# Kernel optimization log

Hardware: AMD Instinct MI355X
Metric: run time of the kernel (lower is better)

The kernel has to match this reference:

```python
import jax, jax.numpy as jnp
import numpy as np
from jax import lax

DIVISOR = 2.0

def setup_inputs() -> dict:
    key = jax.random.key(0)
    k1, k2, k3, k4 = jax.random.split(key, 4)
    x = jax.random.normal(k1, (32, 3, 32, 128, 128), dtype=jnp.float16)
    conv_w = jax.random.normal(k2, (16, 3, 3, 3, 3), dtype=jnp.float16) * 0.1
    conv_b = jax.random.normal(k3, (16,), dtype=jnp.float16)
    bias = jax.random.normal(k4, (16,), dtype=jnp.float16)
    return {"x": x, "conv_w": conv_w, "conv_b": conv_b, "bias": bias}

def reference(x, conv_w, conv_b, bias):
    # Conv3d (valid padding, stride 1), fp16 like conv.half()
    y = lax.conv_general_dilated(
        x, conv_w, window_strides=(1, 1, 1), padding="VALID",
        dimension_numbers=("NCDHW", "OIDHW", "NCDHW"))
    y = y + conv_b[None, :, None, None, None]
    # Fused ReLU + 2x2x2 max pool
    y = jnp.maximum(y, jnp.asarray(0, y.dtype))
    B, C, D, H, W = y.shape
    Dp, Hp, Wp = D // 2, H // 2, W // 2
    pooled = y[:, :, :2 * Dp, :2 * Hp, :2 * Wp].reshape(
        B, C, Dp, 2, Hp, 2, Wp, 2).max(axis=(3, 5, 7))  # [B,C,Dp,Hp,Wp]
    # Spatial mean in fp32 (kernel accumulates in float)
    avg = pooled.astype(jnp.float32).mean(axis=(2, 3, 4))  # [B,C]
    # /divisor + bias[c], then sum over channels -> [B,1,1,1]
    per_ch = avg / DIVISOR + bias.astype(jnp.float32)[None, :]
    return per_ch.sum(axis=1).reshape(B, 1, 1, 1)
```

## Files before the change

### kernel.cpp

```cpp
#include <hip/hip_runtime.h>
#include <hip/hip_bf16.h>


typedef __attribute__((ext_vector_type(8)))  short  short8;
typedef __attribute__((ext_vector_type(4)))  float  floatx4;
typedef __attribute__((ext_vector_type(16))) float  floatx16;

__device__ __forceinline__ short f2bf(float f) {
    unsigned u = __builtin_bit_cast(unsigned, f);
    unsigned r = (u + 0x7FFFu + ((u >> 16) & 1u)) >> 16;
    return (short)r;
}

__device__ __forceinline__ unsigned pkbf2(float a, float b) {
    __hip_bfloat162 h = __float22bfloat162_rn(float2{a, b});
    unsigned r;
    __builtin_memcpy(&r, &h, 4);
    return r;
}

template <int CTRL>
__device__ __forceinline__ float dpp_max(float v) {
    int x = __builtin_bit_cast(int, v);
    int y = __builtin_amdgcn_mov_dpp(x, CTRL, 0xF, 0xF, true);
    return fmaxf(v, __builtin_bit_cast(float, y));
}

__global__ void init_kernel(const float* __restrict__ wg,
                            const float* __restrict__ biasg,
                            short* __restrict__ wtab,
                            float* __restrict__ out)
{
    const int t = threadIdx.x;
    if (t < 576) {
        const int lane = t & 63, f = t >> 6;
        const int kh = f / 3, kw = f % 3;
        const int m = lane & 31, hs = lane >> 5;
        const int dd = m >> 4, ch = m & 15;
        short8 v;
        #pragma unroll
        for (int j = 0; j < 8; ++j) {
            const int s = hs * 8 + j;
            const int dl = s >> 2, ci = s & 3;
            const int kd = dl - dd;
            v[j] = (ci < 3 && kd >= 0 && kd < 3)
                 ? f2bf(wg[ch * 81 + ci * 27 + kd * 9 + kh * 3 + kw]) : (short)0;
        }
        ((short8*)wtab)[f * 64 + lane] = v;
    }
    if (t < 32) {
        float s = 0.f;
        #pragma unroll
        for (int cc = 0; cc < 16; ++cc) s += biasg[cc];
        out[t] = s;
    }
}

__global__ __launch_bounds__(512, 4) void fused_conv_pool_reduce(
    const float* __restrict__ xg,
    const short* __restrict__ wtab,
    const float* __restrict__ cbg,
    float* __restrict__ out)
{
    __shared__ __align__(16) short rawT[2 * 130 * 64];
    __shared__ float wsums[8];

    const int hp  = blockIdx.x;
    const int b   = blockIdx.y;
    const int tid = threadIdx.x;
    const int lane = tid & 63;
    const int wv   = tid >> 6;
    const int hs   = lane >> 5;

    short8 af[9];
    #pragma unroll
    for (int f = 0; f < 9; ++f) af[f] = ((const short8*)wtab)[f * 64 + lane];
    float cb8[8];
    #pragma unroll
    for (int r = 0; r < 8; ++r) cb8[r] = cbg[(r & 3) + 8 * (r >> 2) + 4 * hs];

    if (tid < 64)
        *(unsigned long long*)((char*)rawT + (tid >> 5) * 16640 + 16384 + (tid & 31) * 8) = 0ULL;

    const int w4 = tid & 31, dr = (tid >> 5) & 3, hr = (tid >> 7) & 3;
    int waddr[4];
    {
        const int chunkL = hr * 2 + (dr >> 1);
        #pragma unroll
        for (int i = 0; i < 4; ++i) {
            const int row = 4 * w4 + i;
            const int phys = chunkL ^ ((row ^ (row >> 3)) & 7);
            waddr[i] = row * 128 + phys * 16 + (dr & 1) * 8;
        }
    }
    const int wi = (lane >> 1) & 15, hh = lane & 1;
    int raddr[3][3];
    #pragma unroll
    for (int kh = 0; kh < 3; ++kh) {
        #pragma unroll
        for (int kw = 0; kw < 3; ++kw) {
            const int row = wv * 16 + wi + kw;
            const int phys = ((hh + kh) * 2 + hs) ^ ((row ^ (row >> 3)) & 7);
            raddr[kh][kw] = row * 128 + phys * 16;
        }
    }

    const float* src = xg + ((size_t)b * 96 + dr) * 16384 + (2 * hp + hr) * 128 + 4 * w4;
    floatx4 c0 = *(const floatx4*)(src);
    floatx4 c1 = *(const floatx4*)(src + 524288);
    floatx4 c2 = *(const floatx4*)(src + 1048576);

    float vsum = 0.f;
    for (int dp = 0; dp < 15; ++dp) {
        const int bofs = (dp & 1) * 16640;
        #pragma unroll
        for (int i = 0; i < 4; ++i) {
            uint2 pk;
            pk.x = pkbf2(c0[i], c1[i]);
            pk.y = pkbf2(c2[i], 0.0f);
            *(uint2*)((char*)rawT + bofs + waddr[i]) = pk;
        }
        if (dp < 14) {
            src += 32768;
            c0 = *(const floatx4*)(src);
            c1 = *(const floatx4*)(src + 524288);
            c2 = *(const floatx4*)(src + 1048576);
        }
        __syncthreads();

        floatx16 acc = {0.f,0.f,0.f,0.f,0.f,0.f,0.f,0.f,
                        0.f,0.f,0.f,0.f,0.f,0.f,0.f,0.f};
        #pragma unroll
        for (int kh = 0; kh < 3; ++kh) {
            #pragma unroll
            for (int kw = 0; kw < 3; ++kw) {
                const short8 bf = *(const short8*)((char*)rawT + bofs + raddr[kh][kw]);
                acc = __builtin_amdgcn_mfma_f32_32x32x16_bf16(af[kh * 3 + kw], bf, acc, 0, 0, 0);
            }
        }
        #pragma unroll
        for (int r = 0; r < 8; ++r) {
            float v = fmaxf(fmaxf(acc[r], acc[r + 8]) + cb8[r], 0.f);
            v = dpp_max<0xB1>(v);
            v = dpp_max<0x4E>(v);
            vsum += v;
        }
    }

    const bool okl = ((lane & 3) == 0) && (wv * 16 + wi <= 124);
    float s = okl ? vsum : 0.f;
    #pragma unroll
    for (int off = 1; off < 64; off <<= 1) s += __shfl_xor(s, off, 64);

    if (lane == 0) wsums[wv] = s;
    __syncthreads();
    if (tid == 0) {
        float bs = 0.f;
        #pragma unroll
        for (int i = 0; i < 8; ++i) bs += wsums[i];
        atomicAdd(&out[b], bs * (1.0f / 119070.0f));
    }
}

extern "C" void kernel_launch(void* const* d_in, const int* in_sizes, int n_in,
                              void* d_out, int out_size, void* d_ws, size_t ws_size,
                              hipStream_t stream) {
    const float* x      = (const float*)d_in[0];
    const float* conv_w = (const float*)d_in[1];
    const float* conv_b = (const float*)d_in[2];
    const float* bias   = (const float*)d_in[3];
    float* out = (float*)d_out;
    short* wtab = (short*)d_ws;

    init_kernel<<<1, 576, 0, stream>>>(conv_w, bias, wtab, out);
    dim3 grid(63, 32);
    fused_conv_pool_reduce<<<grid, 512, 0, stream>>>(x, wtab, conv_b, out);
}
```

Before: 302.6 us.

## Deepen global prefetch to two slabs, use raw LDS barrier, remap block order

```diff
diff --git a/kernel.cpp b/kernel.cpp
--- a/kernel.cpp
+++ b/kernel.cpp
@@ -25,6 +25,8 @@
     int y = __builtin_amdgcn_mov_dpp(x, CTRL, 0xF, 0xF, true);
     return fmaxf(v, __builtin_bit_cast(float, y));
 }
+
+#define BAR() asm volatile("s_waitcnt lgkmcnt(0)\n\ts_barrier" ::: "memory")
 
 __global__ void init_kernel(const float* __restrict__ wg,
                             const float* __restrict__ biasg,
@@ -65,8 +67,11 @@
     __shared__ __align__(16) short rawT[2 * 130 * 64];
     __shared__ float wsums[8];
 
-    const int hp  = blockIdx.x;
-    const int b   = blockIdx.y;
+    const int lin = blockIdx.y * 63 + blockIdx.x;
+    const int nl  = (lin & 7) * 252 + (lin >> 3);
+    const int hp  = nl % 63;
+    const int b   = nl / 63;
+
     const int tid = threadIdx.x;
     const int lane = tid & 63;
     const int wv   = tid >> 6;
@@ -105,14 +110,9 @@
         }
     }
 
-    const float* src = xg + ((size_t)b * 96 + dr) * 16384 + (2 * hp + hr) * 128 + 4 * w4;
-    floatx4 c0 = *(const floatx4*)(src);
-    floatx4 c1 = *(const floatx4*)(src + 524288);
-    floatx4 c2 = *(const floatx4*)(src + 1048576);
-
     float vsum = 0.f;
-    for (int dp = 0; dp < 15; ++dp) {
-        const int bofs = (dp & 1) * 16640;
+
+    auto stage = [&](const floatx4& c0, const floatx4& c1, const floatx4& c2, int bofs) {
         #pragma unroll
         for (int i = 0; i < 4; ++i) {
             uint2 pk;
@@ -120,14 +120,8 @@
             pk.y = pkbf2(c2[i], 0.0f);
             *(uint2*)((char*)rawT + bofs + waddr[i]) = pk;
         }
-        if (dp < 14) {
-            src += 32768;
-            c0 = *(const floatx4*)(src);
-            c1 = *(const floatx4*)(src + 524288);
-            c2 = *(const floatx4*)(src + 1048576);
-        }
-        __syncthreads();
-
+    };
+    auto compute = [&](int bofs) {
         floatx16 acc = {0.f,0.f,0.f,0.f,0.f,0.f,0.f,0.f,
                         0.f,0.f,0.f,0.f,0.f,0.f,0.f,0.f};
         #pragma unroll
@@ -145,7 +139,40 @@
             v = dpp_max<0x4E>(v);
             vsum += v;
         }
-    }
+    };
+
+    const float* src = xg + ((size_t)b * 96 + dr) * 16384 + (2 * hp + hr) * 128 + 4 * w4;
+    floatx4 a0 = *(const floatx4*)(src);
+    floatx4 a1 = *(const floatx4*)(src + 524288);
+    floatx4 a2 = *(const floatx4*)(src + 1048576);
+    src += 32768;
+    floatx4 b0 = *(const floatx4*)(src);
+    floatx4 b1 = *(const floatx4*)(src + 524288);
+    floatx4 b2 = *(const floatx4*)(src + 1048576);
+    src += 32768;
+
+    for (int dpb = 0; dpb < 7; ++dpb) {
+        stage(a0, a1, a2, 0);
+        a0 = *(const floatx4*)(src);
+        a1 = *(const floatx4*)(src + 524288);
+        a2 = *(const floatx4*)(src + 1048576);
+        src += 32768;
+        BAR();
+        compute(0);
+
+        stage(b0, b1, b2, 16640);
+        if (dpb < 6) {
+            b0 = *(const floatx4*)(src);
+            b1 = *(const floatx4*)(src + 524288);
+            b2 = *(const floatx4*)(src + 1048576);
+            src += 32768;
+        }
+        BAR();
+        compute(16640);
+    }
+    stage(a0, a1, a2, 0);
+    BAR();
+    compute(0);
 
     const bool okl = ((lane & 3) == 0) && (wv * 16 + wi <= 124);
     float s = okl ? vsum : 0.f;
```

New measurement: 303.5 us. About the same (+0.3%).

## Swap MFMA operands, reorganize LDS ping-pong layout and remap block order

Applied to the files above, without the earlier changes.

```diff
diff --git a/kernel.cpp b/kernel.cpp
--- a/kernel.cpp
+++ b/kernel.cpp
@@ -3,6 +3,7 @@
 
 
 typedef __attribute__((ext_vector_type(8)))  short  short8;
+typedef __attribute__((ext_vector_type(2)))  float  floatx2;
 typedef __attribute__((ext_vector_type(4)))  float  floatx4;
 typedef __attribute__((ext_vector_type(16))) float  floatx16;
 
@@ -25,6 +26,10 @@
     int y = __builtin_amdgcn_mov_dpp(x, CTRL, 0xF, 0xF, true);
     return fmaxf(v, __builtin_bit_cast(float, y));
 }
+
+#define BAR() asm volatile("s_waitcnt lgkmcnt(0)\n\ts_barrier" ::: "memory")
+
+#define BUFSZ 16640
 
 __global__ void init_kernel(const float* __restrict__ wg,
                             const float* __restrict__ biasg,
@@ -36,7 +41,7 @@
         const int lane = t & 63, f = t >> 6;
         const int kh = f / 3, kw = f % 3;
         const int m = lane & 31, hs = lane >> 5;
-        const int dd = m >> 4, ch = m & 15;
+        const int ch = m >> 1, dd = m & 1;
         short8 v;
         #pragma unroll
         for (int j = 0; j < 8; ++j) {
@@ -65,8 +70,11 @@
     __shared__ __align__(16) short rawT[2 * 130 * 64];
     __shared__ float wsums[8];
 
-    const int hp  = blockIdx.x;
-    const int b   = blockIdx.y;
+    const int lin = blockIdx.y * 63 + blockIdx.x;
+    const int nl  = (lin & 7) * 252 + (lin >> 3);
+    const int hp  = nl % 63;
+    const int b   = nl / 63;
+
     const int tid = threadIdx.x;
     const int lane = tid & 63;
     const int wv   = tid >> 6;
@@ -75,24 +83,27 @@
     short8 af[9];
     #pragma unroll
     for (int f = 0; f < 9; ++f) af[f] = ((const short8*)wtab)[f * 64 + lane];
-    float cb8[8];
-    #pragma unroll
-    for (int r = 0; r < 8; ++r) cb8[r] = cbg[(r & 3) + 8 * (r >> 2) + 4 * hs];
+    const float cbv = cbg[(lane >> 1) & 15];
+    float maskA[4];
+    #pragma unroll
+    for (int a = 0; a < 4; ++a) {
+        const bool ok = ((lane & 1) == 0) && (wv * 8 + 2 * a + hs <= 62);
+        maskA[a] = ok ? 1.0f : 0.0f;
+    }
 
     if (tid < 64)
-        *(unsigned long long*)((char*)rawT + (tid >> 5) * 16640 + 16384 + (tid & 31) * 8) = 0ULL;
-
-    const int w4 = tid & 31, dr = (tid >> 5) & 3, hr = (tid >> 7) & 3;
-    int waddr[4];
-    {
-        const int chunkL = hr * 2 + (dr >> 1);
-        #pragma unroll
-        for (int i = 0; i < 4; ++i) {
-            const int row = 4 * w4 + i;
-            const int phys = chunkL ^ ((row ^ (row >> 3)) & 7);
-            waddr[i] = row * 128 + phys * 16 + (dr & 1) * 8;
-        }
-    }
+        *(unsigned long long*)((char*)rawT + (tid >> 5) * BUFSZ + 16384 + (tid & 31) * 8) = 0ULL;
+
+    #define SWZ(r) (((r) ^ ((r) >> 3)) & 7)
+
+    const int w4 = tid & 31, dr2 = (tid >> 5) & 1, rr = (tid >> 6) & 1, hr2 = (tid >> 7) & 3;
+    int waddr2[2];
+    #pragma unroll
+    for (int j = 0; j < 2; ++j) {
+        const int row = 2 * w4 + 64 * rr + j;
+        waddr2[j] = row * 128 + ((hr2 * 2) ^ SWZ(row)) * 16 + dr2 * 8;
+    }
+
     const int wi = (lane >> 1) & 15, hh = lane & 1;
     int raddr[3][3];
     #pragma unroll
@@ -100,33 +111,55 @@
         #pragma unroll
         for (int kw = 0; kw < 3; ++kw) {
             const int row = wv * 16 + wi + kw;
-            const int phys = ((hh + kh) * 2 + hs) ^ ((row ^ (row >> 3)) & 7);
+            const int phys = ((hh + kh) * 2 + hs) ^ SWZ(row);
             raddr[kh][kw] = row * 128 + phys * 16;
         }
     }
 
-    const float* src = xg + ((size_t)b * 96 + dr) * 16384 + (2 * hp + hr) * 128 + 4 * w4;
-    floatx4 c0 = *(const floatx4*)(src);
-    floatx4 c1 = *(const floatx4*)(src + 524288);
-    floatx4 c2 = *(const floatx4*)(src + 1048576);
-
-    float vsum = 0.f;
-    for (int dp = 0; dp < 15; ++dp) {
-        const int bofs = (dp & 1) * 16640;
+    {
+        const int w4p = tid & 31, drp = (tid >> 5) & 3, hrp = (tid >> 7) & 3;
+        const float* srcP = xg + ((size_t)b * 96 + drp) * 16384 + (2 * hp + hrp) * 128 + 4 * w4p;
+        const floatx4 c0 = *(const floatx4*)(srcP);
+        const floatx4 c1 = *(const floatx4*)(srcP + 524288);
+        const floatx4 c2 = *(const floatx4*)(srcP + 1048576);
+        const int chunkL = hrp * 2 + (drp >> 1);
         #pragma unroll
         for (int i = 0; i < 4; ++i) {
+            const int row = 4 * w4p + i;
+            const int ad = row * 128 + (chunkL ^ SWZ(row)) * 16 + (drp & 1) * 8;
             uint2 pk;
             pk.x = pkbf2(c0[i], c1[i]);
             pk.y = pkbf2(c2[i], 0.0f);
-            *(uint2*)((char*)rawT + bofs + waddr[i]) = pk;
-        }
-        if (dp < 14) {
-            src += 32768;
-            c0 = *(const floatx4*)(src);
-            c1 = *(const floatx4*)(src + 524288);
-            c2 = *(const floatx4*)(src + 1048576);
-        }
-        __syncthreads();
+            *(uint2*)((char*)rawT + ad) = pk;
+        }
+    }
+
+    const float* src2 = xg + ((size_t)b * 96 + 4 + dr2) * 16384
+                      + (2 * hp + hr2) * 128 + 2 * w4 + 64 * rr;
+    floatx2 A0 = *(const floatx2*)(src2);
+    floatx2 A1 = *(const floatx2*)(src2 + 524288);
+    floatx2 A2 = *(const floatx2*)(src2 + 1048576);
+
+    float vsum = 0.f;
+    for (int dp = 0; dp < 15; ++dp) {
+        const int p16 = (dp & 1) << 4;
+        if (dp <= 13) {
+            const int bw = (((dp >> 1) + 1) & 1) * BUFSZ;
+            uint2 pk0, pk1;
+            pk0.x = pkbf2(A0[0], A1[0]); pk0.y = pkbf2(A2[0], 0.0f);
+            pk1.x = pkbf2(A0[1], A1[1]); pk1.y = pkbf2(A2[1], 0.0f);
+            *(uint2*)((char*)rawT + bw + (waddr2[0] ^ p16)) = pk0;
+            *(uint2*)((char*)rawT + bw + (waddr2[1] ^ p16)) = pk1;
+            if (dp <= 12) {
+                src2 += 32768;
+                A0 = *(const floatx2*)(src2);
+                A1 = *(const floatx2*)(src2 + 524288);
+                A2 = *(const floatx2*)(src2 + 1048576);
+            }
+        }
+        BAR();
+
+        const int roff = (((dp + hs) >> 1) & 1) * BUFSZ;
 
         floatx16 acc = {0.f,0.f,0.f,0.f,0.f,0.f,0.f,0.f,
                         0.f,0.f,0.f,0.f,0.f,0.f,0.f,0.f};
@@ -134,21 +167,22 @@
         for (int kh = 0; kh < 3; ++kh) {
             #pragma unroll
             for (int kw = 0; kw < 3; ++kw) {
-                const short8 bf = *(const short8*)((char*)rawT + bofs + raddr[kh][kw]);
-                acc = __builtin_amdgcn_mfma_f32_32x32x16_bf16(af[kh * 3 + kw], bf, acc, 0, 0, 0);
+                const short8 bf = *(const short8*)((char*)rawT + roff + (raddr[kh][kw] ^ p16));
+                acc = __builtin_amdgcn_mfma_f32_32x32x16_bf16(bf, af[kh * 3 + kw], acc, 0, 0, 0);
             }
         }
         #pragma unroll
-        for (int r = 0; r < 8; ++r) {
-            float v = fmaxf(fmaxf(acc[r], acc[r + 8]) + cb8[r], 0.f);
-            v = dpp_max<0xB1>(v);
-            v = dpp_max<0x4E>(v);
-            vsum += v;
-        }
-    }
-
-    const bool okl = ((lane & 3) == 0) && (wv * 16 + wi <= 124);
-    float s = okl ? vsum : 0.f;
+        for (int a = 0; a < 4; ++a) {
+            float m01 = fmaxf(acc[4 * a],     acc[4 * a + 1]);
+            float m23 = fmaxf(acc[4 * a + 2], acc[4 * a + 3]);
+            float m   = fmaxf(m01, m23);
+            m = dpp_max<0xB1>(m);
+            const float v = fmaxf(m + cbv, 0.f);
+            vsum = fmaf(maskA[a], v, vsum);
+        }
+    }
+
+    float s = vsum;
     #pragma unroll
     for (int off = 1; off < 64; off <<= 1) s += __shfl_xor(s, off, 64);
 
```

Measured after the change: 287.2 us, median of 2. -5.1%, faster.
